# Kernel tuning notes

Hardware: AMD Instinct MI355X
Metric: run time of the kernel (lower is better)

Reference implementation:

```python
import jax, jax.numpy as jnp
import numpy as np

B, H, L, V = 128, 1024, 60, 50257


def setup_inputs() -> dict:
    key = jax.random.key(0)
    ks = jax.random.split(key, 14)
    s = 0.02
    f32 = jnp.float32
    return {
        "input": jax.random.randint(ks[0], (B,), 0, V),
        "hidden": jax.random.normal(ks[1], (1, B, H), f32),
        "encoder_outputs": jax.random.normal(ks[2], (B, L, H), f32),
        # learned parameters
        "emb": (jax.random.normal(ks[3], (V, H), f32) * s),
        "attn_W": (jax.random.normal(ks[4], (L, 2 * H), f32) * s),
        "attn_b": jnp.zeros((L,), f32),
        "comb_W": (jax.random.normal(ks[5], (H, 2 * H), f32) * s),
        "comb_b": jnp.zeros((H,), f32),
        "W_ih": (jax.random.normal(ks[6], (3 * H, H), f32) * s),
        "W_hh": (jax.random.normal(ks[7], (3 * H, H), f32) * s),
        "b_ih": jnp.zeros((3 * H,), f32),
        "b_hh": jnp.zeros((3 * H,), f32),
        "out_W": (jax.random.normal(ks[8], (V, H), f32) * s),
        "out_b": jnp.zeros((V,), f32),
    }


def reference(input, hidden, encoder_outputs, emb, attn_W, attn_b,
              comb_W, comb_b, W_ih, W_hh, b_ih, b_hh, out_W, out_b):
    # embedding lookup (dropout is identity in eval mode)
    embedded = emb[input]                      # [B, H]
    h = hidden[0]                              # [B, H]

    # Bahdanau-style attention over fixed max_length positions
    attn_logits = jnp.concatenate([embedded, h], axis=1) @ attn_W.T + attn_b  # [B, L]
    attn_weights = jax.nn.softmax(attn_logits, axis=1)                        # [B, L]
    attn_applied = jnp.einsum('bl,blh->bh', attn_weights, encoder_outputs)    # [B, H]

    # combine + relu
    x = jnp.concatenate([embedded, attn_applied], axis=1) @ comb_W.T + comb_b  # [B, H]
    x = jax.nn.relu(x)

    # single GRU step (PyTorch gate order: r, z, n)
    gi = x @ W_ih.T + b_ih                     # [B, 3H]
    gh = h @ W_hh.T + b_hh                     # [B, 3H]
    i_r, i_z, i_n = jnp.split(gi, 3, axis=1)
    h_r, h_z, h_n = jnp.split(gh, 3, axis=1)
    r = jax.nn.sigmoid(i_r + h_r)
    z = jax.nn.sigmoid(i_z + h_z)
    n = jnp.tanh(i_n + r * h_n)
    h_new = (1.0 - z) * n + z * h              # [B, H]

    # output projection + log_softmax over vocab
    logp = jax.nn.log_softmax(h_new @ out_W.T + out_b, axis=1)  # [B, V]
    return logp, h_new[None], attn_weights
```

## Files before the change

### kernel.cpp

```cpp
#include <hip/hip_runtime.h>
#include <hip/hip_bf16.h>

#define B_ 128
#define H_ 1024
#define L_ 60
#define V_ 50257

typedef __attribute__((ext_vector_type(8))) short bf16x8;
typedef __attribute__((ext_vector_type(4))) float f32x4;

__device__ __forceinline__ unsigned short f2bf(float f) {
  union { __hip_bfloat16 h; unsigned short u; } v;
  v.h = __float2bfloat16(f);
  return v.u;
}

__device__ __forceinline__ bf16x8 cvt8(float4 a, float4 b) {
  union { bf16x8 v; __hip_bfloat16 h[8]; } u;
  u.h[0] = __float2bfloat16(a.x); u.h[1] = __float2bfloat16(a.y);
  u.h[2] = __float2bfloat16(a.z); u.h[3] = __float2bfloat16(a.w);
  u.h[4] = __float2bfloat16(b.x); u.h[5] = __float2bfloat16(b.y);
  u.h[6] = __float2bfloat16(b.z); u.h[7] = __float2bfloat16(b.w);
  return u.v;
}

__device__ __forceinline__ void gl_lds16(const void* g, void* l) {
  __builtin_amdgcn_global_load_lds(
      (const __attribute__((address_space(1))) unsigned int*)g,
      (__attribute__((address_space(3))) unsigned int*)l, 16, 0, 0);
}

#define SBAR()   __builtin_amdgcn_s_barrier()
#define SCHED0() __builtin_amdgcn_sched_barrier(0)
__device__ __forceinline__ void vwait4() { asm volatile("s_waitcnt vmcnt(4)" ::: "memory"); }
__device__ __forceinline__ void vwait0() { asm volatile("s_waitcnt vmcnt(0)" ::: "memory"); }

__device__ __forceinline__ size_t packIdx(int b, int k) {
  int s = k >> 5;
  int bm = b >> 4;
  int lane = (b & 15) | (((k >> 3) & 3) << 4);
  return ((size_t)((s * 8 + bm) * 64 + lane) << 3) | (size_t)(k & 7);
}

__global__ __launch_bounds__(256) void k_embh(
    const int* __restrict__ input, const float* __restrict__ hidden,
    const float* __restrict__ emb, unsigned short* __restrict__ aXa,
    unsigned short* __restrict__ aH)
{
  int idx = blockIdx.x * 256 + threadIdx.x;
  int b = idx >> 10, j = idx & (H_ - 1);
  float e = emb[(size_t)input[b] * H_ + j];
  float h = hidden[idx];
  size_t p = packIdx(b, j);
  aXa[p] = f2bf(e);
  aH[p]  = f2bf(h);
}

__global__ __launch_bounds__(256) void k_alog(
    const int* __restrict__ input, const float* __restrict__ hidden,
    const float* __restrict__ emb, const float* __restrict__ attn_W,
    const float* __restrict__ attn_b, float* __restrict__ lbuf)
{
  int t = threadIdx.x, wv = t >> 6, lane = t & 63;
  int task = blockIdx.x * 4 + wv;
  int b = task / L_, l = task - b * L_;
  const float* erow = emb + (size_t)input[b] * H_;
  const float* hrow = hidden + (size_t)b * H_;
  const float* wr = attn_W + (size_t)l * (2 * H_);
  float acc = 0.f;
  #pragma unroll 4
  for (int i = 0; i < 16; ++i) {
    int m = lane + i * 64;
    acc += erow[m] * wr[m] + hrow[m] * wr[H_ + m];
  }
  #pragma unroll
  for (int off = 32; off; off >>= 1) acc += __shfl_xor(acc, off);
  if (lane == 0) lbuf[b * 64 + l] = acc + attn_b[l];
}

__global__ __launch_bounds__(256) void k_asm(
    const float* __restrict__ lbuf, float* __restrict__ attnw,
    float* __restrict__ wbuf)
{
  int t = threadIdx.x, wv = t >> 6, lane = t & 63;
  int b = blockIdx.x * 4 + wv;
  float v = (lane < L_) ? lbuf[b * 64 + lane] : -1e30f;
  float m = v;
  #pragma unroll
  for (int off = 32; off; off >>= 1) m = fmaxf(m, __shfl_xor(m, off));
  float e = (lane < L_) ? __expf(v - m) : 0.f;
  float s = e;
  #pragma unroll
  for (int off = 32; off; off >>= 1) s += __shfl_xor(s, off);
  float w = e / s;
  if (lane < L_) { attnw[b * L_ + lane] = w; wbuf[b * 64 + lane] = w; }
}

__global__ __launch_bounds__(256) void k_app(
    const float* __restrict__ enc, const float* __restrict__ wbuf,
    unsigned short* __restrict__ aXa)
{
  __shared__ float sWt[64];
  int b = blockIdx.x, q = blockIdx.y, t = threadIdx.x;
  if (t < L_) sWt[t] = wbuf[b * 64 + t];
  __syncthreads();
  int col = q * 256 + t;
  const float* eb = enc + (size_t)b * L_ * H_ + col;
  float acc = 0.f;
  #pragma unroll 4
  for (int l = 0; l < L_; ++l) acc += sWt[l] * eb[(size_t)l * H_];
  aXa[packIdx(b, H_ + col)] = f2bf(acc);
}

__global__ __launch_bounds__(256) void k_gemm(
    const unsigned short* __restrict__ Apk, const unsigned short* __restrict__ Apk2,
    const float* __restrict__ Wt, const float* __restrict__ Wt2,
    const float* __restrict__ bias, float* __restrict__ Cdir,
    float* __restrict__ Cpart, float* __restrict__ Cpart2,
    float* __restrict__ pms, int K, int N, int nchunks, int halfY, int nblkx)
{
  __shared__ __align__(16) float bufW[3][64 * 32];
  __shared__ __align__(16) unsigned short bufA[3][128 * 32];
  int t = threadIdx.x, wv = t >> 6, lane = t & 63;
  int y = blockIdx.y;
  const unsigned short* A = Apk;
  const float* W = Wt;
  float* CP = Cpart;
  int sidx = y;
  if (halfY && y >= halfY) { A = Apk2; W = Wt2; CP = Cpart2; sidx = y - halfY; }
  int chunk0 = sidx * nchunks;
  int n0 = blockIdx.x * 64;
  int bm0 = wv * 2;
  int srow8 = lane >> 3;
  int sch = lane & 7;

  f32x4 acc[2][4];
  #pragma unroll
  for (int i = 0; i < 2; ++i)
    #pragma unroll
    for (int j = 0; j < 4; ++j) acc[i][j] = (f32x4){0.f, 0.f, 0.f, 0.f};

  auto STAGE = [&](int kc, int bi) {
    #pragma unroll
    for (int i = 0; i < 2; ++i) {
      int r = wv * 16 + i * 8 + srow8;
      int gcol = n0 + r; gcol = (gcol < N) ? gcol : (N - 1);
      int c = sch ^ (r & 7);
      const float* src = W + (size_t)gcol * K + (size_t)kc * 32 + c * 4;
      gl_lds16(src, &bufW[bi][(wv * 16 + i * 8) * 32]);
    }
    #pragma unroll
    for (int j = 0; j < 2; ++j) {
      const unsigned short* src = A + ((size_t)kc * 8 + bm0 + j) * 512 + lane * 8;
      gl_lds16(src, &bufA[bi][(bm0 + j) * 512]);
    }
  };

  STAGE(chunk0, 0);
  STAGE(chunk0 + 1, 1);

  int g = lane >> 4;
  int bi = 0;
  for (int kk = 0; kk < nchunks; ++kk) {
    if (kk < nchunks - 1) vwait4(); else vwait0();
    SCHED0(); SBAR(); SCHED0();
    if (kk + 2 < nchunks) {
      int bi2 = bi + 2; if (bi2 >= 3) bi2 -= 3;
      STAGE(chunk0 + kk + 2, bi2);
    }
    const float* bw = bufW[bi];
    const unsigned short* ba = bufA[bi];
    bf16x8 a0 = *(const bf16x8*)&ba[(bm0) * 512 + lane * 8];
    bf16x8 a1 = *(const bf16x8*)&ba[(bm0 + 1) * 512 + lane * 8];
    #pragma unroll
    for (int nc = 0; nc < 4; ++nc) {
      int rr = nc * 16 + (lane & 15);
      int c0 = (g * 2) ^ (rr & 7);
      int c1 = (g * 2 + 1) ^ (rr & 7);
      float4 w0 = *(const float4*)&bw[rr * 32 + c0 * 4];
      float4 w1 = *(const float4*)&bw[rr * 32 + c1 * 4];
      bf16x8 bfr = cvt8(w0, w1);
      acc[0][nc] = __builtin_amdgcn_mfma_f32_16x16x32_bf16(a0, bfr, acc[0][nc], 0, 0, 0);
      acc[1][nc] = __builtin_amdgcn_mfma_f32_16x16x32_bf16(a1, bfr, acc[1][nc], 0, 0, 0);
    }
    bi = (bi == 2) ? 0 : bi + 1;
  }

  int cols[4]; float bv[4];
  #pragma unroll
  for (int nc = 0; nc < 4; ++nc) {
    int c = n0 + nc * 16 + (lane & 15);
    cols[nc] = c;
    bv[nc] = (bias && c < N) ? bias[c] : 0.f;
  }
  int rb = (lane >> 4) * 4;
  if (CP) {
    float* dst = CP + (size_t)sidx * B_ * N;
    #pragma unroll
    for (int bm = 0; bm < 2; ++bm)
      #pragma unroll
      for (int r = 0; r < 4; ++r) {
        int row = (bm0 + bm) * 16 + rb + r;
        #pragma unroll
        for (int nc = 0; nc < 4; ++nc)
          if (cols[nc] < N) dst[(size_t)row * N + cols[nc]] = acc[bm][nc][r];
      }
  } else {
    #pragma unroll
    for (int bm = 0; bm < 2; ++bm)
      #pragma unroll
      for (int r = 0; r < 4; ++r) {
        int row = (bm0 + bm) * 16 + rb + r;
        #pragma unroll
        for (int nc = 0; nc < 4; ++nc)
          if (cols[nc] < N) Cdir[(size_t)row * N + cols[nc]] = acc[bm][nc][r] + bv[nc];
      }
    if (pms) {
      #pragma unroll
      for (int bm = 0; bm < 2; ++bm)
        #pragma unroll
        for (int r = 0; r < 4; ++r) {
          int row = (bm0 + bm) * 16 + rb + r;
          float m = -1e30f;
          #pragma unroll
          for (int nc = 0; nc < 4; ++nc)
            if (cols[nc] < N) m = fmaxf(m, acc[bm][nc][r] + bv[nc]);
          #pragma unroll
          for (int off = 8; off; off >>= 1) m = fmaxf(m, __shfl_xor(m, off));
          float e = 0.f;
          #pragma unroll
          for (int nc = 0; nc < 4; ++nc)
            if (cols[nc] < N) e += __expf(acc[bm][nc][r] + bv[nc] - m);
          #pragma unroll
          for (int off = 8; off; off >>= 1) e += __shfl_xor(e, off);
          if ((lane & 15) == 0) {
            size_t o = ((size_t)row * nblkx + blockIdx.x) * 2;
            pms[o] = m; pms[o + 1] = e;
          }
        }
    }
  }
}

__global__ __launch_bounds__(256) void k_reduce_comb(
    const float* __restrict__ parts, const float* __restrict__ bias,
    unsigned short* __restrict__ aX)
{
  int idx = blockIdx.x * 256 + threadIdx.x;
  int b = idx >> 10, j = idx & (H_ - 1);
  float s = bias[j];
  #pragma unroll
  for (int p = 0; p < 16; ++p) s += parts[(size_t)p * B_ * H_ + idx];
  s = fmaxf(s, 0.f);
  aX[packIdx(b, j)] = f2bf(s);
}

__global__ __launch_bounds__(256) void k_gate(
    const float* __restrict__ giP, const float* __restrict__ ghP,
    const float* __restrict__ b_ih, const float* __restrict__ b_hh,
    const float* __restrict__ hidden, float* __restrict__ hnew,
    unsigned short* __restrict__ aHn)
{
  int idx = blockIdx.x * 256 + threadIdx.x;
  int b = idx >> 10, j = idx & (H_ - 1);
  size_t base = (size_t)b * 3 * H_;
  float ir = b_ih[j], iz = b_ih[H_ + j], in_ = b_ih[2 * H_ + j];
  float hr = b_hh[j], hz = b_hh[H_ + j], hn = b_hh[2 * H_ + j];
  #pragma unroll
  for (int p = 0; p < 4; ++p) {
    const float* gi = giP + (size_t)p * B_ * 3 * H_ + base;
    const float* gh = ghP + (size_t)p * B_ * 3 * H_ + base;
    ir += gi[j]; iz += gi[H_ + j]; in_ += gi[2 * H_ + j];
    hr += gh[j]; hz += gh[H_ + j]; hn += gh[2 * H_ + j];
  }
  float r = 1.f / (1.f + __expf(-(ir + hr)));
  float z = 1.f / (1.f + __expf(-(iz + hz)));
  float n = tanhf(in_ + r * hn);
  float h = hidden[idx];
  float hv = (1.f - z) * n + z * h;
  hnew[idx] = hv;
  aHn[packIdx(b, j)] = f2bf(hv);
}

#define SL_ 6283
__global__ __launch_bounds__(256) void k_lsub(
    float* __restrict__ logits, const float* __restrict__ pms, int nblk)
{
  __shared__ float sm[4], ss[4], sc;
  int b = blockIdx.x, sl = blockIdx.y, t = threadIdx.x;
  float M = -1e30f, S = 0.f;
  for (int i = t; i < nblk; i += 256) {
    float m = pms[((size_t)b * nblk + i) * 2];
    float s = pms[((size_t)b * nblk + i) * 2 + 1];
    float nm = fmaxf(M, m);
    S = S * __expf(M - nm) + s * __expf(m - nm);
    M = nm;
  }
  #pragma unroll
  for (int off = 32; off; off >>= 1) {
    float m2 = __shfl_xor(M, off), s2 = __shfl_xor(S, off);
    float nm = fmaxf(M, m2);
    S = S * __expf(M - nm) + s2 * __expf(m2 - nm);
    M = nm;
  }
  if ((t & 63) == 0) { sm[t >> 6] = M; ss[t >> 6] = S; }
  __syncthreads();
  if (t == 0) {
    float Mf = sm[0], Sf = ss[0];
    #pragma unroll
    for (int i = 1; i < 4; ++i) {
      float nm = fmaxf(Mf, sm[i]);
      Sf = Sf * __expf(Mf - nm) + ss[i] * __expf(sm[i] - nm);
      Mf = nm;
    }
    sc = Mf + logf(Sf);
  }
  __syncthreads();
  float c = sc;
  int v0 = sl * SL_;
  int v1 = v0 + SL_; if (v1 > V_) v1 = V_;
  float* row = logits + (size_t)b * V_;
  for (int v = v0 + t; v < v1; v += 256) row[v] -= c;
}

extern "C" void kernel_launch(void* const* d_in, const int* in_sizes, int n_in,
                              void* d_out, int out_size, void* d_ws, size_t ws_size,
                              hipStream_t stream)
{
  const int*   input  = (const int*)d_in[0];
  const float* hidden = (const float*)d_in[1];
  const float* enc    = (const float*)d_in[2];
  const float* emb    = (const float*)d_in[3];
  const float* attn_W = (const float*)d_in[4];
  const float* attn_b = (const float*)d_in[5];
  const float* comb_W = (const float*)d_in[6];
  const float* comb_b = (const float*)d_in[7];
  const float* W_ih   = (const float*)d_in[8];
  const float* W_hh   = (const float*)d_in[9];
  const float* b_ih   = (const float*)d_in[10];
  const float* b_hh   = (const float*)d_in[11];
  const float* out_W  = (const float*)d_in[12];
  const float* out_b  = (const float*)d_in[13];

  float* out    = (float*)d_out;
  float* logits = out;
  float* hnew   = out + (size_t)B_ * V_;
  float* attnw  = hnew + (size_t)B_ * H_;

  const int NBLK = (V_ + 63) / 64;
  char* ws = (char*)d_ws;
  unsigned short* aXa = (unsigned short*)(ws);
  unsigned short* aH  = (unsigned short*)(ws + 524288);
  unsigned short* aX  = (unsigned short*)(ws + 786432);
  unsigned short* aHn = (unsigned short*)(ws + 1048576);
  float* wbuf  = (float*)(ws + 1310720);
  float* lbuf  = (float*)(ws + 1343488);
  float* pms   = (float*)(ws + 1376256);
  float* combP = (float*)(ws + 2185216);
  float* giP   = (float*)(ws + 2185216);
  float* ghP   = (float*)(ws + 2185216 + 6291456);

  k_embh<<<512, 256, 0, stream>>>(input, hidden, emb, aXa, aH);
  k_alog<<<(B_ * L_) / 4, 256, 0, stream>>>(input, hidden, emb, attn_W, attn_b, lbuf);
  k_asm<<<B_ / 4, 256, 0, stream>>>(lbuf, attnw, wbuf);
  k_app<<<dim3(B_, 4), 256, 0, stream>>>(enc, wbuf, aXa);
  k_gemm<<<dim3(16, 16), 256, 0, stream>>>(aXa, nullptr, comb_W, nullptr, nullptr,
                                           nullptr, combP, nullptr, nullptr,
                                           2 * H_, H_, 4, 0, 0);
  k_reduce_comb<<<(B_ * H_) / 256, 256, 0, stream>>>(combP, comb_b, aX);
  k_gemm<<<dim3(48, 8), 256, 0, stream>>>(aX, aH, W_ih, W_hh, nullptr,
                                          nullptr, giP, ghP, nullptr,
                                          H_, 3 * H_, 8, 4, 0);
  k_gate<<<(B_ * H_) / 256, 256, 0, stream>>>(giP, ghP, b_ih, b_hh, hidden, hnew, aHn);
  k_gemm<<<dim3(NBLK, 1), 256, 0, stream>>>(aHn, nullptr, out_W, nullptr, out_b,
                                            logits, nullptr, nullptr, pms,
                                            H_, V_, 32, 0, NBLK);
  k_lsub<<<dim3(B_, 8), 256, 0, stream>>>(logits, pms, NBLK);
}
```

Measured before the change: 147.9 us.

## Load A fragments directly to registers and double-buffer W in LDS

Restructures the k_gemm main loop from a 3-stage LDS ring holding both W and A tiles to a 2-buffer ping-pong for W only. The A (bf16 packed activations) fragments now load straight from global memory into registers, and launch bounds request 6 blocks per CU. The aim is to cut LDS footprint and traffic to raise occupancy. In exchange the pipeline is shallower, there are more barriers per chunk, and register pressure is higher. The loop assumes nchunks is even; an odd count would read one chunk past the block's range.

After: 135.1 us. 8.6% less time.

```diff
diff --git a/kernel.cpp b/kernel.cpp
--- a/kernel.cpp
+++ b/kernel.cpp
@@ -112,15 +112,15 @@
   aXa[packIdx(b, H_ + col)] = f2bf(acc);
 }
 
-__global__ __launch_bounds__(256) void k_gemm(
+__global__ __launch_bounds__(256, 6) void k_gemm(
     const unsigned short* __restrict__ Apk, const unsigned short* __restrict__ Apk2,
     const float* __restrict__ Wt, const float* __restrict__ Wt2,
     const float* __restrict__ bias, float* __restrict__ Cdir,
     float* __restrict__ Cpart, float* __restrict__ Cpart2,
     float* __restrict__ pms, int K, int N, int nchunks, int halfY, int nblkx)
 {
-  __shared__ __align__(16) float bufW[3][64 * 32];
-  __shared__ __align__(16) unsigned short bufA[3][128 * 32];
+  __shared__ __align__(16) float bufW0[64 * 32];
+  __shared__ __align__(16) float bufW1[64 * 32];
   int t = threadIdx.x, wv = t >> 6, lane = t & 63;
   int y = blockIdx.y;
   const unsigned short* A = Apk;
@@ -133,6 +133,7 @@
   int bm0 = wv * 2;
   int srow8 = lane >> 3;
   int sch = lane & 7;
+  int g = lane >> 4;
 
   f32x4 acc[2][4];
   #pragma unroll
@@ -140,38 +141,22 @@
     #pragma unroll
     for (int j = 0; j < 4; ++j) acc[i][j] = (f32x4){0.f, 0.f, 0.f, 0.f};
 
-  auto STAGE = [&](int kc, int bi) {
+  auto SW = [&](int kc, float* buf) {
     #pragma unroll
     for (int i = 0; i < 2; ++i) {
       int r = wv * 16 + i * 8 + srow8;
       int gcol = n0 + r; gcol = (gcol < N) ? gcol : (N - 1);
       int c = sch ^ (r & 7);
       const float* src = W + (size_t)gcol * K + (size_t)kc * 32 + c * 4;
-      gl_lds16(src, &bufW[bi][(wv * 16 + i * 8) * 32]);
-    }
-    #pragma unroll
-    for (int j = 0; j < 2; ++j) {
-      const unsigned short* src = A + ((size_t)kc * 8 + bm0 + j) * 512 + lane * 8;
-      gl_lds16(src, &bufA[bi][(bm0 + j) * 512]);
+      gl_lds16(src, buf + (wv * 16 + i * 8) * 32);
     }
   };
-
-  STAGE(chunk0, 0);
-  STAGE(chunk0 + 1, 1);
-
-  int g = lane >> 4;
-  int bi = 0;
-  for (int kk = 0; kk < nchunks; ++kk) {
-    if (kk < nchunks - 1) vwait4(); else vwait0();
-    SCHED0(); SBAR(); SCHED0();
-    if (kk + 2 < nchunks) {
-      int bi2 = bi + 2; if (bi2 >= 3) bi2 -= 3;
-      STAGE(chunk0 + kk + 2, bi2);
-    }
-    const float* bw = bufW[bi];
-    const unsigned short* ba = bufA[bi];
-    bf16x8 a0 = *(const bf16x8*)&ba[(bm0) * 512 + lane * 8];
-    bf16x8 a1 = *(const bf16x8*)&ba[(bm0 + 1) * 512 + lane * 8];
+  const bf16x8* apg = (const bf16x8*)A;
+  auto LA = [&](int kc, bf16x8& x0, bf16x8& x1) {
+    x0 = apg[((size_t)kc * 8 + bm0) * 64 + lane];
+    x1 = apg[((size_t)kc * 8 + bm0 + 1) * 64 + lane];
+  };
+  auto COMP = [&](const float* bw, bf16x8 a0, bf16x8 a1) {
     #pragma unroll
     for (int nc = 0; nc < 4; ++nc) {
       int rr = nc * 16 + (lane & 15);
@@ -183,7 +168,26 @@
       acc[0][nc] = __builtin_amdgcn_mfma_f32_16x16x32_bf16(a0, bfr, acc[0][nc], 0, 0, 0);
       acc[1][nc] = __builtin_amdgcn_mfma_f32_16x16x32_bf16(a1, bfr, acc[1][nc], 0, 0, 0);
     }
-    bi = (bi == 2) ? 0 : bi + 1;
+  };
+
+  bf16x8 aA0, aA1, aB0, aB1;
+  SW(chunk0, bufW0);     LA(chunk0, aA0, aA1);
+  SW(chunk0 + 1, bufW1); LA(chunk0 + 1, aB0, aB1);
+  vwait4(); SCHED0(); SBAR();
+
+  for (int kk = 0; kk < nchunks; kk += 2) {
+    COMP(bufW0, aA0, aA1);
+    SCHED0(); SBAR();
+    if (kk + 2 < nchunks) { SW(chunk0 + kk + 2, bufW0); LA(chunk0 + kk + 2, aA0, aA1); vwait4(); }
+    else vwait0();
+    SCHED0(); SBAR();
+    COMP(bufW1, aB0, aB1);
+    if (kk + 2 < nchunks) {
+      SCHED0(); SBAR();
+      if (kk + 3 < nchunks) { SW(chunk0 + kk + 3, bufW1); LA(chunk0 + kk + 3, aB0, aB1); vwait4(); }
+      else vwait0();
+      SCHED0(); SBAR();
+    }
   }
 
   int cols[4]; float bv[4];
```
